# Kernel optimization log

Measured on AMD Instinct MI355X. Metric: run time of the kernel, lower is better.

Reference implementation:

```python
import jax, jax.numpy as jnp
import numpy as np

B, S, D, H, L = 8, 1024, 768, 12, 12
HD = D // H          # head dim 64
F = 4 * D            # mlp hidden 3072
N_SEG = 8            # ~images packed per sequence


def layer_norm(x, w, b, eps=1e-5):
    m = jnp.mean(x, axis=-1, keepdims=True)
    v = jnp.mean((x - m) ** 2, axis=-1, keepdims=True)
    return (x - m) / jnp.sqrt(v + eps) * w + b


def setup_inputs() -> dict:
    key = jax.random.key(0)
    ks = jax.random.split(key, 16)
    packed_tokens = jax.random.normal(ks[0], (B, S, D), dtype=jnp.float32)
    # block-diagonal mask from sorted segment ids (True = disallowed, torch bool-mask convention)
    seg = jnp.sort(jax.random.randint(ks[1], (S,), 0, N_SEG))
    attn_mask = seg[:, None] != seg[None, :]
    std = 0.02
    p = {
        'packed_tokens': packed_tokens,
        'attn_mask': attn_mask,
        'ln1_w': jnp.ones((L, D), jnp.float32),
        'ln1_b': jnp.zeros((L, D), jnp.float32),
        'wqkv': jax.random.normal(ks[2], (L, D, 3 * D), jnp.float32) * std,
        'bqkv': jnp.zeros((L, 3 * D), jnp.float32),
        'wo': jax.random.normal(ks[3], (L, D, D), jnp.float32) * std,
        'bo': jnp.zeros((L, D), jnp.float32),
        'ln2_w': jnp.ones((L, D), jnp.float32),
        'ln2_b': jnp.zeros((L, D), jnp.float32),
        'w1': jax.random.normal(ks[4], (L, D, F), jnp.float32) * std,
        'b1': jnp.zeros((L, F), jnp.float32),
        'w2': jax.random.normal(ks[5], (L, F, D), jnp.float32) * std,
        'b2': jnp.zeros((L, D), jnp.float32),
        'norm_w': jnp.ones((D,), jnp.float32),
        'norm_b': jnp.zeros((D,), jnp.float32),
    }
    return p


def attention(x, mask, wqkv, bqkv, wo, bo):
    qkv = x @ wqkv + bqkv                                  # [B,S,3D]
    q, k, v = jnp.split(qkv, 3, axis=-1)
    q = q.reshape(B, S, H, HD)
    k = k.reshape(B, S, H, HD)
    v = v.reshape(B, S, H, HD)
    scores = jnp.einsum('bqhd,bkhd->bhqk', q, k) / jnp.sqrt(jnp.asarray(HD, x.dtype))
    neg = jnp.asarray(jnp.finfo(scores.dtype).min, scores.dtype)
    scores = jnp.where(mask[None, None], neg, scores)
    probs = jax.nn.softmax(scores, axis=-1)
    out = jnp.einsum('bhqk,bkhd->bqhd', probs, v).reshape(B, S, D)
    return out @ wo + bo


def reference(packed_tokens, attn_mask, ln1_w, ln1_b, wqkv, bqkv, wo, bo,
              ln2_w, ln2_b, w1, b1, w2, b2, norm_w, norm_b):
    x = packed_tokens  # dropout = identity in eval
    for l in range(L):
        n = layer_norm(x, ln1_w[l], ln1_b[l])
        x = x + attention(n, attn_mask, wqkv[l], bqkv[l], wo[l], bo[l])
        n = layer_norm(x, ln2_w[l], ln2_b[l])
        h = jax.nn.gelu(n @ w1[l] + b1[l], approximate=False)
        x = x + h @ w2[l] + b2[l]
    return layer_norm(x, norm_w, norm_b)
```

## Files before the change

kernel.cpp:

```cpp
#include <hip/hip_runtime.h>
#include <hip/hip_bf16.h>
#include <math.h>

typedef __hip_bfloat16 bf16_t;
typedef _Float16 h16;
typedef _Float16 f16x8 __attribute__((ext_vector_type(8)));
typedef float f32x4 __attribute__((ext_vector_type(4)));

constexpr int B = 8;
constexpr int S = 1024;
constexpr int D = 768;
constexpr int H = 12;
constexpr int HD = 64;
constexpr int F = 3072;
constexpr int L = 12;
constexpr int T = B * S;


typedef const __attribute__((address_space(1))) void g_void;
typedef __attribute__((address_space(3))) void s_void;
#define GLD16(gp, lp) __builtin_amdgcn_global_load_lds((g_void*)(gp), (s_void*)(lp), 16, 0, 0)

__device__ __forceinline__ float ldf(const void* p, size_t i, int f32) {
    return f32 ? ((const float*)p)[i] : __bfloat162float(((const bf16_t*)p)[i]);
}

__device__ __forceinline__ int xcd_swz(int orig, int nwg) {
    return (orig & 7) * (nwg >> 3) + (orig >> 3);
}

__global__ void dtype_sniff_kernel(const uint32_t* __restrict__ w, int* __restrict__ meta) {
    if (threadIdx.x == 0) meta[1] = (w[0] == 0x3F800000u) ? 1 : 0;
}

__global__ __launch_bounds__(256) void mask_sniff_kernel(const uint32_t* __restrict__ mask,
                                                         int* __restrict__ meta) {
    __shared__ int firstw;
    if (threadIdx.x == 0) firstw = 1 << 30;
    __syncthreads();
    int idx = threadIdx.x;
    uint32_t v0 = mask[idx];
    uint32_t v1 = mask[256 + idx];
    uint32_t v2 = mask[512 + idx];
    uint32_t v3 = mask[768 + idx];
    int best = 1 << 30;
    if (v3) best = 768 + idx;
    if (v2) best = 512 + idx;
    if (v1) best = 256 + idx;
    if (v0) best = idx;
    atomicMin(&firstw, best);
    __syncthreads();
    if (threadIdx.x == 0) {
        int fi = firstw;
        meta[0] = (fi < (1 << 30) && mask[fi] == 1u) ? 1 : 0;
    }
}

__global__ __launch_bounds__(256) void rowrange_kernel(const void* __restrict__ mask,
                                                       int* __restrict__ meta) {
    int q = blockIdx.x;
    int f = meta[0];
    int lo = S, hi = -1;
    for (int j = threadIdx.x; j < S; j += 256) {
        int v = f ? ((const int*)mask)[(size_t)q * S + j]
                  : (int)((const unsigned char*)mask)[(size_t)q * S + j];
        if (v == 0) { lo = min(lo, j); hi = max(hi, j); }
    }
    for (int off = 32; off > 0; off >>= 1) {
        lo = min(lo, __shfl_xor(lo, off));
        hi = max(hi, __shfl_xor(hi, off));
    }
    __shared__ int slo[4], shi[4];
    int wv = threadIdx.x >> 6;
    if ((threadIdx.x & 63) == 0) { slo[wv] = lo; shi[wv] = hi; }
    __syncthreads();
    if (threadIdx.x == 0) {
        lo = min(min(slo[0], slo[1]), min(slo[2], slo[3]));
        hi = max(max(shi[0], shi[1]), max(shi[2], shi[3]));
        if (lo > hi) { lo = q; hi = q; }
        meta[16 + q] = lo;
        meta[16 + S + q] = hi;
    }
}

__global__ __launch_bounds__(256) void cast_kernel(const void* __restrict__ in,
                                                   const int* __restrict__ meta,
                                                   float* __restrict__ out, int n) {
    int f32 = meta[1];
    int i = blockIdx.x * 256 + threadIdx.x;
    if (i < n) out[i] = ldf(in, i, f32);
}

template <bool EXTERNAL>
__global__ __launch_bounds__(256) void ln_kernel(const float* __restrict__ x,
                                                 const void* __restrict__ w, size_t wo_,
                                                 const void* __restrict__ b, size_t bo_,
                                                 const int* __restrict__ meta,
                                                 void* __restrict__ out) {
    int f32 = meta[1];
    int t = blockIdx.x;
    int tid = threadIdx.x;
    __shared__ float xs[D];
    __shared__ float red[16];
    const float* xp = x + (size_t)t * D;

    float s = 0.f;
#pragma unroll
    for (int i = 0; i < 3; i++) {
        float v = xp[tid + i * 256];
        xs[tid + i * 256] = v;
        s += v;
    }
    for (int off = 32; off > 0; off >>= 1) s += __shfl_xor(s, off);
    int wv = tid >> 6, lane = tid & 63;
    if (lane == 0) red[wv] = s;
    __syncthreads();
    float mean = (red[0] + red[1] + red[2] + red[3]) * (1.0f / 768.0f);

    float s2 = 0.f;
#pragma unroll
    for (int i = 0; i < 3; i++) {
        float d = xs[tid + i * 256] - mean;
        s2 += d * d;
    }
    for (int off = 32; off > 0; off >>= 1) s2 += __shfl_xor(s2, off);
    if (lane == 0) red[8 + wv] = s2;
    __syncthreads();
    float var = (red[8] + red[9] + red[10] + red[11]) * (1.0f / 768.0f);
    float rstd = rsqrtf(var + 1e-5f);

#pragma unroll
    for (int i = 0; i < 3; i++) {
        int d = tid + i * 256;
        float v = (xs[d] - mean) * rstd * ldf(w, wo_ + d, f32) + ldf(b, bo_ + d, f32);
        size_t idx = (size_t)t * D + d;
        if (EXTERNAL) {
            if (f32) ((float*)out)[idx] = v;
            else ((bf16_t*)out)[idx] = __float2bfloat16(v);
        } else {
            ((h16*)out)[idx] = (h16)v;
        }
    }
}

__global__ __launch_bounds__(256) void wtrans_kernel(const void* __restrict__ W, size_t woff,
                                                     const int* __restrict__ meta,
                                                     h16* __restrict__ wt,
                                                     int K, int N) {
    int f32 = meta[1];
    __shared__ float tile[32][33];
    int n0 = blockIdx.x * 32, k0 = blockIdx.y * 32;
    int tx = threadIdx.x & 31, ty = threadIdx.x >> 5;
#pragma unroll
    for (int i = 0; i < 4; i++) {
        int k = ty + i * 8;
        tile[k][tx] = ldf(W, woff + (size_t)(k0 + k) * N + n0 + tx, f32);
    }
    __syncthreads();
#pragma unroll
    for (int i = 0; i < 4; i++) {
        int nn = ty + i * 8;
        wt[(size_t)(n0 + nn) * K + k0 + tx] = (h16)tile[tx][nn];
    }
}

template <bool GELU, bool ADD>
__global__ __launch_bounds__(256) void mgemm_kernel(const h16* __restrict__ A,
                                                    const h16* __restrict__ Bt,
                                                    const void* __restrict__ bias, size_t boff,
                                                    const int* __restrict__ meta,
                                                    void* __restrict__ C,
                                                    int M, int N, int K) {
    int f32 = meta[1];
    __shared__ h16 smem[4][128 * 32];
    int tid = threadIdx.x;
    int lane = tid & 63;
    int wv = tid >> 6;
    int wy = wv >> 1, wx = wv & 1;

    int nwg = gridDim.x * gridDim.y;
    int orig = blockIdx.y * gridDim.x + blockIdx.x;
    int fid = xcd_swz(orig, nwg);
    int n0 = (fid % gridDim.x) * 128;
    int m0 = (fid / gridDim.x) * 128;

    int row0 = tid >> 2;
    int row1 = 64 + row0;
    int kbs = ((tid & 3) ^ ((tid >> 3) & 3)) * 8;
    const h16* ag0 = A + (size_t)(m0 + row0) * K + kbs;
    const h16* ag1 = A + (size_t)(m0 + row1) * K + kbs;
    const h16* bg0 = Bt + (size_t)(n0 + row0) * K + kbs;
    const h16* bg1 = Bt + (size_t)(n0 + row1) * K + kbs;

    int arow = lane & 15;
    int akb = ((lane >> 4) ^ ((arow >> 1) & 3)) * 8;
    int aoff = (wy * 64 + arow) * 32 + akb;
    int boff2 = (wx * 64 + arow) * 32 + akb;

    f32x4 acc[4][4];
#pragma unroll
    for (int i = 0; i < 4; i++)
#pragma unroll
        for (int j = 0; j < 4; j++) acc[i][j] = (f32x4){0.f, 0.f, 0.f, 0.f};

    int nst = K >> 5;
    GLD16(ag0, &smem[0][(size_t)tid * 8]);
    GLD16(ag1, &smem[0][(size_t)(256 + tid) * 8]);
    GLD16(bg0, &smem[2][(size_t)tid * 8]);
    GLD16(bg1, &smem[2][(size_t)(256 + tid) * 8]);
    __syncthreads();

    int cur = 0;
    for (int t = 0; t < nst; ++t) {
        if (t + 1 < nst) {
            int nb = cur ^ 1;
            int off = (t + 1) * 32;
            GLD16(ag0 + off, &smem[nb][(size_t)tid * 8]);
            GLD16(ag1 + off, &smem[nb][(size_t)(256 + tid) * 8]);
            GLD16(bg0 + off, &smem[2 + nb][(size_t)tid * 8]);
            GLD16(bg1 + off, &smem[2 + nb][(size_t)(256 + tid) * 8]);
        }
        const h16* pa = &smem[cur][aoff];
        const h16* pb = &smem[2 + cur][boff2];
        f16x8 af[4], bf[4];
#pragma unroll
        for (int i = 0; i < 4; i++) af[i] = *(const f16x8*)(pa + i * 16 * 32);
#pragma unroll
        for (int j = 0; j < 4; j++) bf[j] = *(const f16x8*)(pb + j * 16 * 32);
#pragma unroll
        for (int i = 0; i < 4; i++)
#pragma unroll
            for (int j = 0; j < 4; j++)
                acc[i][j] = __builtin_amdgcn_mfma_f32_16x16x32_f16(af[i], bf[j], acc[i][j], 0, 0, 0);
        __syncthreads();
        cur ^= 1;
    }

    int col_local = wx * 64 + (lane & 15);
    int row_local = wy * 64 + (lane >> 4) * 4;
    if (ADD) {
#pragma unroll
        for (int j = 0; j < 4; j++) {
            int nn = n0 + col_local + j * 16;
            float bv = ldf(bias, boff + nn, f32);
#pragma unroll
            for (int i = 0; i < 4; i++) {
#pragma unroll
                for (int r = 0; r < 4; r++) {
                    int mm = m0 + row_local + i * 16 + r;
                    float v = acc[i][j][r] + bv;
                    ((float*)C)[(size_t)mm * N + nn] += v;
                }
            }
        }
    } else {
        h16* cst = &smem[0][0];
#pragma unroll
        for (int j = 0; j < 4; j++) {
            int cl = col_local + j * 16;
            float bv = ldf(bias, boff + n0 + cl, f32);
#pragma unroll
            for (int i = 0; i < 4; i++) {
#pragma unroll
                for (int r = 0; r < 4; r++) {
                    int rl = row_local + i * 16 + r;
                    float v = acc[i][j][r] + bv;
                    if (GELU) v = 0.5f * v * (1.0f + erff(v * 0.70710678118654752f));
                    cst[rl * 128 + (cl ^ ((rl & 7) << 3))] = (h16)v;
                }
            }
        }
        __syncthreads();
        int row = tid >> 1, cb = (tid & 1) * 64;
        h16* cg = (h16*)C + (size_t)(m0 + row) * N + n0 + cb;
#pragma unroll
        for (int u = 0; u < 8; u++) {
            int ce = cb + u * 8;
            f16x8 vv = *(const f16x8*)&cst[row * 128 + (ce ^ ((row & 7) << 3))];
            *(f16x8*)(cg + u * 8) = vv;
        }
    }
}

template <bool GELU, bool ADD>
__global__ __launch_bounds__(256) void gemm_kernel(const h16* __restrict__ A,
                                                   const void* __restrict__ W, size_t wo_,
                                                   const void* __restrict__ bias, size_t bo_,
                                                   const int* __restrict__ meta,
                                                   void* __restrict__ C,
                                                   int M, int N, int K) {
    int f32 = meta[1];
    __shared__ float As[16][65];
    __shared__ float Bs[16][65];
    int tid = threadIdx.y * 16 + threadIdx.x;
    int m0 = blockIdx.y * 64, n0 = blockIdx.x * 64;
    float c[4][4] = {};

    for (int k0 = 0; k0 < K; k0 += 16) {
#pragma unroll
        for (int i = 0; i < 4; i++) {
            int flat = tid + i * 256;
            int m = flat >> 4, k = flat & 15;
            As[k][m] = (float)A[(size_t)(m0 + m) * K + k0 + k];
        }
#pragma unroll
        for (int i = 0; i < 4; i++) {
            int flat = tid + i * 256;
            int k = flat >> 6, n = flat & 63;
            Bs[k][n] = ldf(W, wo_ + (size_t)(k0 + k) * N + n0 + n, f32);
        }
        __syncthreads();
#pragma unroll
        for (int kk = 0; kk < 16; kk++) {
            float a[4], bb[4];
#pragma unroll
            for (int i = 0; i < 4; i++) a[i] = As[kk][threadIdx.y * 4 + i];
#pragma unroll
            for (int j = 0; j < 4; j++) bb[j] = Bs[kk][threadIdx.x * 4 + j];
#pragma unroll
            for (int i = 0; i < 4; i++)
#pragma unroll
                for (int j = 0; j < 4; j++) c[i][j] += a[i] * bb[j];
        }
        __syncthreads();
    }

#pragma unroll
    for (int i = 0; i < 4; i++) {
        int m = m0 + threadIdx.y * 4 + i;
#pragma unroll
        for (int j = 0; j < 4; j++) {
            int n = n0 + threadIdx.x * 4 + j;
            float v = c[i][j] + ldf(bias, bo_ + n, f32);
            if (GELU) v = 0.5f * v * (1.0f + erff(v * 0.70710678118654752f));
            size_t idx = (size_t)m * N + n;
            if (ADD) ((float*)C)[idx] += v;
            else ((h16*)C)[idx] = (h16)v;
        }
    }
}

__global__ __launch_bounds__(256) void mattn_kernel(const h16* __restrict__ qkv,
                                                    const int* __restrict__ meta,
                                                    h16* __restrict__ ao) {
    const int* rowlo = meta + 16;
    const int* rowhi = meta + 16 + S;

    int nwg = gridDim.x * gridDim.y;
    int orig = blockIdx.y * gridDim.x + blockIdx.x;
    int fid = xcd_swz(orig, nwg);
    int bh = fid / gridDim.x;
    int q0 = (fid % gridDim.x) * 64;

    int b = bh / H, h = bh % H;
    int tid = threadIdx.x;
    int lane = tid & 63;
    int w = tid >> 6;
    int qw = q0 + w * 16;

    __shared__ h16 Vt[64 * 64];
    __shared__ h16 Ps[4][16 * 64];

    const size_t rs = 3 * D;
    const h16* base = qkv + (size_t)b * S * rs;

    int rl = rowlo[q0 + lane], rh = rowhi[q0 + lane];
    for (int off = 32; off > 0; off >>= 1) {
        rl = min(rl, __shfl_xor(rl, off));
        rh = max(rh, __shfl_xor(rh, off));
    }
    int c_lo = rl & ~63;
    int c_hi = rh + 1;

    int qrow = qw + (lane >> 4) * 4;
    int mlo[4], mhi[4];
#pragma unroll
    for (int r = 0; r < 4; r++) { mlo[r] = rowlo[qrow + r]; mhi[r] = rowhi[qrow + r]; }

    f16x8 qf[2];
    {
        const h16* qp = base + (size_t)(qw + (lane & 15)) * rs + h * 64 + (lane >> 4) * 8;
        qf[0] = *(const f16x8*)(qp);
        qf[1] = *(const f16x8*)(qp + 32);
    }

    float m_r[4], l_r[4];
    f32x4 o[4];
#pragma unroll
    for (int r = 0; r < 4; r++) { m_r[r] = -1e30f; l_r[r] = 0.f; }
#pragma unroll
    for (int jf = 0; jf < 4; jf++) o[jf] = (f32x4){0.f, 0.f, 0.f, 0.f};

    for (int c0 = c_lo; c0 < c_hi; c0 += 64) {
        {
            int k = tid & 63, d0 = (tid >> 6) * 16;
            const h16* vp = base + (size_t)(c0 + k) * rs + 2 * D + h * 64 + d0;
            f16x8 v0 = *(const f16x8*)vp;
            f16x8 v1 = *(const f16x8*)(vp + 8);
#pragma unroll
            for (int j = 0; j < 8; j++) {
                int d = d0 + j;
                Vt[(d * 64 + k) ^ ((d & 7) << 3)] = v0[j];
                d = d0 + 8 + j;
                Vt[(d * 64 + k) ^ ((d & 7) << 3)] = v1[j];
            }
        }

        f32x4 s[4];
#pragma unroll
        for (int jf = 0; jf < 4; jf++) {
            const h16* kp = base + (size_t)(c0 + jf * 16 + (lane & 15)) * rs + D + h * 64 + (lane >> 4) * 8;
            f16x8 kf0 = *(const f16x8*)kp;
            f16x8 kf1 = *(const f16x8*)(kp + 32);
            s[jf] = (f32x4){0.f, 0.f, 0.f, 0.f};
            s[jf] = __builtin_amdgcn_mfma_f32_16x16x32_f16(qf[0], kf0, s[jf], 0, 0, 0);
            s[jf] = __builtin_amdgcn_mfma_f32_16x16x32_f16(qf[1], kf1, s[jf], 0, 0, 0);
        }

        float pmax[4];
#pragma unroll
        for (int r = 0; r < 4; r++) pmax[r] = -3.0e38f;
#pragma unroll
        for (int jf = 0; jf < 4; jf++) {
            int k = c0 + jf * 16 + (lane & 15);
#pragma unroll
            for (int r = 0; r < 4; r++) {
                float v = (k < mlo[r] || k > mhi[r]) ? -3.0e38f : s[jf][r] * 0.125f;
                s[jf][r] = v;
                pmax[r] = fmaxf(pmax[r], v);
            }
        }
#pragma unroll
        for (int off = 1; off < 16; off <<= 1)
#pragma unroll
            for (int r = 0; r < 4; r++) pmax[r] = fmaxf(pmax[r], __shfl_xor(pmax[r], off));

        float scl[4];
#pragma unroll
        for (int r = 0; r < 4; r++) {
            float mn = fmaxf(m_r[r], pmax[r]);
            scl[r] = __expf(m_r[r] - mn);
            m_r[r] = mn;
            l_r[r] *= scl[r];
        }
#pragma unroll
        for (int jf = 0; jf < 4; jf++) {
#pragma unroll
            for (int r = 0; r < 4; r++) {
                float e = __expf(s[jf][r] - m_r[r]);
                l_r[r] += e;
                int q = (lane >> 4) * 4 + r;
                int k = jf * 16 + (lane & 15);
                Ps[w][(q * 64 + k) ^ ((q & 7) << 3)] = (h16)e;
            }
        }
#pragma unroll
        for (int jf = 0; jf < 4; jf++)
#pragma unroll
            for (int r = 0; r < 4; r++) o[jf][r] *= scl[r];

        __syncthreads();

        f16x8 pa0, pa1;
        {
            int q = lane & 15;
            int e0 = q * 64 + (lane >> 4) * 8;
            int e1 = q * 64 + 32 + (lane >> 4) * 8;
            pa0 = *(const f16x8*)&Ps[w][e0 ^ ((q & 7) << 3)];
            pa1 = *(const f16x8*)&Ps[w][e1 ^ ((q & 7) << 3)];
        }
#pragma unroll
        for (int jf = 0; jf < 4; jf++) {
            int d = jf * 16 + (lane & 15);
            int e0 = d * 64 + (lane >> 4) * 8;
            int e1 = d * 64 + 32 + (lane >> 4) * 8;
            f16x8 vb0 = *(const f16x8*)&Vt[e0 ^ ((d & 7) << 3)];
            f16x8 vb1 = *(const f16x8*)&Vt[e1 ^ ((d & 7) << 3)];
            o[jf] = __builtin_amdgcn_mfma_f32_16x16x32_f16(pa0, vb0, o[jf], 0, 0, 0);
            o[jf] = __builtin_amdgcn_mfma_f32_16x16x32_f16(pa1, vb1, o[jf], 0, 0, 0);
        }
        __syncthreads();
    }

#pragma unroll
    for (int off = 1; off < 16; off <<= 1)
#pragma unroll
        for (int r = 0; r < 4; r++) l_r[r] += __shfl_xor(l_r[r], off);
#pragma unroll
    for (int jf = 0; jf < 4; jf++) {
        int d = jf * 16 + (lane & 15);
#pragma unroll
        for (int r = 0; r < 4; r++) {
            float inv = (l_r[r] > 0.f) ? 1.0f / l_r[r] : 0.f;
            int q = qw + (lane >> 4) * 4 + r;
            ao[(size_t)(b * S + q) * D + h * 64 + d] = (h16)(o[jf][r] * inv);
        }
    }
}

__global__ __launch_bounds__(512) void attn_kernel(const h16* __restrict__ qkv,
                                                   const int* __restrict__ meta,
                                                   h16* __restrict__ ao) {
    const int* rowlo = meta + 16;
    const int* rowhi = meta + 16 + S;
    int bh = blockIdx.x;
    int b = bh / H, h = bh % H;
    int q0 = blockIdx.y * 8;
    int tid = threadIdx.x;
    int qr = tid >> 6;
    int lane = tid & 63;
    int q = q0 + qr;

    __shared__ float qs[8][64];
    __shared__ float sc[8][S];
    __shared__ float kv[64][65];

    const size_t rowstride = 3 * D;
    const h16* qkv_b = qkv + (size_t)b * S * rowstride;

    qs[qr][lane] = (float)qkv_b[(size_t)(q0 + qr) * rowstride + h * 64 + lane];

    int lo = rowlo[q], hi = rowhi[q];
    int blo = S, bhi = -1;
#pragma unroll
    for (int i = 0; i < 8; i++) {
        blo = min(blo, rowlo[q0 + i]);
        bhi = max(bhi, rowhi[q0 + i]);
    }
    int c_lo = (blo / 64) * 64;
    int c_hi = bhi + 1;
    int c_up = c_lo + ((c_hi - c_lo + 63) / 64) * 64;

    for (int c0 = c_lo; c0 < c_hi; c0 += 64) {
        __syncthreads();
#pragma unroll
        for (int i = 0; i < 8; i++) {
            int flat = tid + i * 512;
            int jj = flat >> 6, dd = flat & 63;
            kv[jj][dd] = (float)qkv_b[(size_t)(c0 + jj) * rowstride + D + h * 64 + dd];
        }
        __syncthreads();
        float acc = 0.f;
#pragma unroll
        for (int d = 0; d < 64; d++) acc += qs[qr][d] * kv[lane][d];
        int j = c0 + lane;
        bool msk = (j < lo) || (j > hi);
        sc[qr][j] = msk ? -3.0e38f : acc * 0.125f;
    }
    __syncthreads();

    float m = -3.4e38f;
    for (int j = c_lo + lane; j < c_up; j += 64) m = fmaxf(m, sc[qr][j]);
    for (int off = 32; off > 0; off >>= 1) m = fmaxf(m, __shfl_xor(m, off));
    float sum = 0.f;
    for (int j = c_lo + lane; j < c_up; j += 64) {
        float e = expf(sc[qr][j] - m);
        sc[qr][j] = e;
        sum += e;
    }
    for (int off = 32; off > 0; off >>= 1) sum += __shfl_xor(sum, off);
    float inv = (sum > 0.f) ? 1.0f / sum : 0.f;

    float out = 0.f;
    for (int c0 = c_lo; c0 < c_hi; c0 += 64) {
        __syncthreads();
#pragma unroll
        for (int i = 0; i < 8; i++) {
            int flat = tid + i * 512;
            int jj = flat >> 6, dd = flat & 63;
            kv[jj][dd] = (float)qkv_b[(size_t)(c0 + jj) * rowstride + 2 * D + h * 64 + dd];
        }
        __syncthreads();
#pragma unroll
        for (int jj = 0; jj < 64; jj++) out += sc[qr][c0 + jj] * kv[jj][lane];
    }
    out *= inv;
    ao[((size_t)(b * S + q)) * D + h * 64 + lane] = (h16)out;
}

__global__ __launch_bounds__(256) void sentinel_kernel(uint32_t* __restrict__ out, int nwords) {
    int i = blockIdx.x * 256 + threadIdx.x;
    if (i < nwords) out[i] = 0x3F803F80u;
}

extern "C" void kernel_launch(void* const* d_in, const int* in_sizes, int n_in,
                              void* d_out, int out_size, void* d_ws, size_t ws_size,
                              hipStream_t stream) {
    const void* packed = d_in[0];
    const void* mask   = d_in[1];
    const void* ln1w   = d_in[2];
    const void* ln1b   = d_in[3];
    const void* wqkv   = d_in[4];
    const void* bqkv   = d_in[5];
    const void* wo     = d_in[6];
    const void* bo     = d_in[7];
    const void* ln2w   = d_in[8];
    const void* ln2b   = d_in[9];
    const void* w1     = d_in[10];
    const void* b1     = d_in[11];
    const void* w2     = d_in[12];
    const void* b2     = d_in[13];
    const void* normw  = d_in[14];
    const void* normb  = d_in[15];

    size_t x_b   = (size_t)T * D * 4;
    size_t n_b   = (size_t)T * D * 2;
    size_t big_b = (size_t)T * F * 2;
    size_t need_old = 16384 + x_b + n_b + big_b;
    size_t wt_elems = (size_t)3 * D * D + (size_t)D * D + (size_t)D * F + (size_t)F * D;
    size_t need_new = need_old + wt_elems * 2 ;

    if (ws_size < need_old) {
        int nwords = out_size / 2;
        sentinel_kernel<<<(nwords + 255) / 256, 256, 0, stream>>>((uint32_t*)d_out, nwords);
        return;
    }

    int* meta = (int*)d_ws;
    float* x  = (float*)((char*)d_ws + 16384);
    h16* n    = (h16*)((char*)x + x_b);
    h16* big  = (h16*)((char*)n + n_b);

    dtype_sniff_kernel<<<1, 64, 0, stream>>>((const uint32_t*)ln1w, meta);
    mask_sniff_kernel<<<1, 256, 0, stream>>>((const uint32_t*)mask, meta);
    rowrange_kernel<<<S, 256, 0, stream>>>(mask, meta);
    cast_kernel<<<(T * D + 255) / 256, 256, 0, stream>>>(packed, meta, x, T * D);

    if (ws_size >= need_new) {
        h16* wts = (h16*)((char*)big + big_b);
        h16* qkvT = wts;
        h16* woT  = qkvT + (size_t)3 * D * D;
        h16* w1T  = woT + (size_t)D * D;
        h16* w2T  = w1T + (size_t)D * F;

        for (int l = 0; l < L; l++) {
            wtrans_kernel<<<dim3(3 * D / 32, D / 32), 256, 0, stream>>>(
                wqkv, (size_t)l * D * 3 * D, meta, qkvT, D, 3 * D);
            wtrans_kernel<<<dim3(D / 32, D / 32), 256, 0, stream>>>(
                wo, (size_t)l * D * D, meta, woT, D, D);
            wtrans_kernel<<<dim3(F / 32, D / 32), 256, 0, stream>>>(
                w1, (size_t)l * D * F, meta, w1T, D, F);
            wtrans_kernel<<<dim3(D / 32, F / 32), 256, 0, stream>>>(
                w2, (size_t)l * F * D, meta, w2T, F, D);

            ln_kernel<false><<<T, 256, 0, stream>>>(x, ln1w, (size_t)l * D, ln1b, (size_t)l * D, meta, n);
            mgemm_kernel<false, false><<<dim3(3 * D / 128, T / 128), 256, 0, stream>>>(
                n, qkvT, bqkv, (size_t)l * 3 * D, meta, big, T, 3 * D, D);
            mattn_kernel<<<dim3(S / 64, B * H), 256, 0, stream>>>(big, meta, n);
            mgemm_kernel<false, true><<<dim3(D / 128, T / 128), 256, 0, stream>>>(
                n, woT, bo, (size_t)l * D, meta, x, T, D, D);
            ln_kernel<false><<<T, 256, 0, stream>>>(x, ln2w, (size_t)l * D, ln2b, (size_t)l * D, meta, n);
            mgemm_kernel<true, false><<<dim3(F / 128, T / 128), 256, 0, stream>>>(
                n, w1T, b1, (size_t)l * F, meta, big, T, F, D);
            mgemm_kernel<false, true><<<dim3(D / 128, T / 128), 256, 0, stream>>>(
                big, w2T, b2, (size_t)l * D, meta, x, T, D, F);
        }
    } else {
        dim3 thr(16, 16);
        for (int l = 0; l < L; l++) {
            ln_kernel<false><<<T, 256, 0, stream>>>(x, ln1w, (size_t)l * D, ln1b, (size_t)l * D, meta, n);
            gemm_kernel<false, false><<<dim3(3 * D / 64, T / 64), thr, 0, stream>>>(
                n, wqkv, (size_t)l * D * 3 * D, bqkv, (size_t)l * 3 * D, meta, big, T, 3 * D, D);
            attn_kernel<<<dim3(B * H, S / 8), 512, 0, stream>>>(big, meta, n);
            gemm_kernel<false, true><<<dim3(D / 64, T / 64), thr, 0, stream>>>(
                n, wo, (size_t)l * D * D, bo, (size_t)l * D, meta, x, T, D, D);
            ln_kernel<false><<<T, 256, 0, stream>>>(x, ln2w, (size_t)l * D, ln2b, (size_t)l * D, meta, n);
            gemm_kernel<true, false><<<dim3(F / 64, T / 64), thr, 0, stream>>>(
                n, w1, (size_t)l * D * F, b1, (size_t)l * F, meta, big, T, F, D);
            gemm_kernel<false, true><<<dim3(D / 64, T / 64), thr, 0, stream>>>(
                big, w2, (size_t)l * F * D, b2, (size_t)l * D, meta, x, T, D, F);
        }
    }
    ln_kernel<true><<<T, 256, 0, stream>>>(x, normw, 0, normb, 0, meta, d_out);
}
```

Baseline: 4.016 ms.

## Widen GEMM N-tile to 256 for QKV/MLP1 and pre-transpose all layer weights

Templates the MFMA GEMM on the number of 16-wide N fragments so the QKV and FC1 GEMMs use 128x256 tiles (more accumulators per wave, more reuse of A fragments), with the epilogue staged through LDS in 128-column passes. It also transposes all layers' weights up front into a larger workspace region when space allows, instead of transposing per layer between dependent kernels. The wider tiles raise register pressure and halve the grid for those GEMMs, which may reduce occupancy; the upfront transpose needs more workspace.

```diff
diff --git a/kernel.cpp b/kernel.cpp
--- a/kernel.cpp
+++ b/kernel.cpp
@@ -164,15 +164,18 @@
     }
 }
 
-template <bool GELU, bool ADD>
+template <bool GELU, bool ADD, int NF>
 __global__ __launch_bounds__(256) void mgemm_kernel(const h16* __restrict__ A,
                                                     const h16* __restrict__ Bt,
                                                     const void* __restrict__ bias, size_t boff,
                                                     const int* __restrict__ meta,
                                                     void* __restrict__ C,
                                                     int M, int N, int K) {
+    constexpr int BN = NF * 32;
+    constexpr int ASZ = 128 * 32;
+    constexpr int BSZ = BN * 32;
     int f32 = meta[1];
-    __shared__ h16 smem[4][128 * 32];
+    __shared__ h16 smem[2 * ASZ + 2 * BSZ];
     int tid = threadIdx.x;
     int lane = tid & 63;
     int wv = tid >> 6;
@@ -181,33 +184,31 @@
     int nwg = gridDim.x * gridDim.y;
     int orig = blockIdx.y * gridDim.x + blockIdx.x;
     int fid = xcd_swz(orig, nwg);
-    int n0 = (fid % gridDim.x) * 128;
+    int n0 = (fid % gridDim.x) * BN;
     int m0 = (fid / gridDim.x) * 128;
 
     int row0 = tid >> 2;
-    int row1 = 64 + row0;
     int kbs = ((tid & 3) ^ ((tid >> 3) & 3)) * 8;
-    const h16* ag0 = A + (size_t)(m0 + row0) * K + kbs;
-    const h16* ag1 = A + (size_t)(m0 + row1) * K + kbs;
-    const h16* bg0 = Bt + (size_t)(n0 + row0) * K + kbs;
-    const h16* bg1 = Bt + (size_t)(n0 + row1) * K + kbs;
+    const h16* ag = A + (size_t)(m0 + row0) * K + kbs;
+    const h16* bg = Bt + (size_t)(n0 + row0) * K + kbs;
 
     int arow = lane & 15;
     int akb = ((lane >> 4) ^ ((arow >> 1) & 3)) * 8;
     int aoff = (wy * 64 + arow) * 32 + akb;
-    int boff2 = (wx * 64 + arow) * 32 + akb;
-
-    f32x4 acc[4][4];
+    int boff2 = (wx * (NF * 16) + arow) * 32 + akb;
+
+    f32x4 acc[4][NF];
 #pragma unroll
     for (int i = 0; i < 4; i++)
 #pragma unroll
-        for (int j = 0; j < 4; j++) acc[i][j] = (f32x4){0.f, 0.f, 0.f, 0.f};
+        for (int j = 0; j < NF; j++) acc[i][j] = (f32x4){0.f, 0.f, 0.f, 0.f};
 
     int nst = K >> 5;
-    GLD16(ag0, &smem[0][(size_t)tid * 8]);
-    GLD16(ag1, &smem[0][(size_t)(256 + tid) * 8]);
-    GLD16(bg0, &smem[2][(size_t)tid * 8]);
-    GLD16(bg1, &smem[2][(size_t)(256 + tid) * 8]);
+    GLD16(ag, smem + (size_t)tid * 8);
+    GLD16(ag + (size_t)64 * K, smem + (size_t)(256 + tid) * 8);
+#pragma unroll
+    for (int i = 0; i < NF / 2; i++)
+        GLD16(bg + (size_t)(i * 64) * K, smem + 2 * ASZ + (size_t)(i * 256 + tid) * 8);
     __syncthreads();
 
     int cur = 0;
@@ -215,69 +216,81 @@
         if (t + 1 < nst) {
             int nb = cur ^ 1;
             int off = (t + 1) * 32;
-            GLD16(ag0 + off, &smem[nb][(size_t)tid * 8]);
-            GLD16(ag1 + off, &smem[nb][(size_t)(256 + tid) * 8]);
-            GLD16(bg0 + off, &smem[2 + nb][(size_t)tid * 8]);
-            GLD16(bg1 + off, &smem[2 + nb][(size_t)(256 + tid) * 8]);
-        }
-        const h16* pa = &smem[cur][aoff];
-        const h16* pb = &smem[2 + cur][boff2];
-        f16x8 af[4], bf[4];
+            GLD16(ag + off, smem + (size_t)nb * ASZ + (size_t)tid * 8);
+            GLD16(ag + (size_t)64 * K + off, smem + (size_t)nb * ASZ + (size_t)(256 + tid) * 8);
+#pragma unroll
+            for (int i = 0; i < NF / 2; i++)
+                GLD16(bg + (size_t)(i * 64) * K + off,
+                      smem + 2 * ASZ + (size_t)nb * BSZ + (size_t)(i * 256 + tid) * 8);
+        }
+        const h16* pa = smem + (size_t)cur * ASZ + aoff;
+        const h16* pb = smem + 2 * ASZ + (size_t)cur * BSZ + boff2;
+        f16x8 af[4];
 #pragma unroll
         for (int i = 0; i < 4; i++) af[i] = *(const f16x8*)(pa + i * 16 * 32);
 #pragma unroll
-        for (int j = 0; j < 4; j++) bf[j] = *(const f16x8*)(pb + j * 16 * 32);
-#pragma unroll
-        for (int i = 0; i < 4; i++)
-#pragma unroll
-            for (int j = 0; j < 4; j++)
-                acc[i][j] = __builtin_amdgcn_mfma_f32_16x16x32_f16(af[i], bf[j], acc[i][j], 0, 0, 0);
+        for (int jh = 0; jh < NF / 4; jh++) {
+            f16x8 bf[4];
+#pragma unroll
+            for (int jj = 0; jj < 4; jj++) bf[jj] = *(const f16x8*)(pb + (jh * 4 + jj) * 16 * 32);
+#pragma unroll
+            for (int i = 0; i < 4; i++)
+#pragma unroll
+                for (int jj = 0; jj < 4; jj++)
+                    acc[i][jh * 4 + jj] =
+                        __builtin_amdgcn_mfma_f32_16x16x32_f16(af[i], bf[jj], acc[i][jh * 4 + jj], 0, 0, 0);
+        }
         __syncthreads();
         cur ^= 1;
     }
 
-    int col_local = wx * 64 + (lane & 15);
     int row_local = wy * 64 + (lane >> 4) * 4;
     if (ADD) {
 #pragma unroll
-        for (int j = 0; j < 4; j++) {
-            int nn = n0 + col_local + j * 16;
+        for (int j = 0; j < NF; j++) {
+            int nn = n0 + wx * (NF * 16) + (lane & 15) + j * 16;
             float bv = ldf(bias, boff + nn, f32);
 #pragma unroll
             for (int i = 0; i < 4; i++) {
 #pragma unroll
                 for (int r = 0; r < 4; r++) {
                     int mm = m0 + row_local + i * 16 + r;
-                    float v = acc[i][j][r] + bv;
-                    ((float*)C)[(size_t)mm * N + nn] += v;
+                    ((float*)C)[(size_t)mm * N + nn] += acc[i][j][r] + bv;
                 }
             }
         }
     } else {
-        h16* cst = &smem[0][0];
-#pragma unroll
-        for (int j = 0; j < 4; j++) {
-            int cl = col_local + j * 16;
-            float bv = ldf(bias, boff + n0 + cl, f32);
-#pragma unroll
-            for (int i = 0; i < 4; i++) {
-#pragma unroll
-                for (int r = 0; r < 4; r++) {
-                    int rl = row_local + i * 16 + r;
-                    float v = acc[i][j][r] + bv;
-                    if (GELU) v = 0.5f * v * (1.0f + erff(v * 0.70710678118654752f));
-                    cst[rl * 128 + (cl ^ ((rl & 7) << 3))] = (h16)v;
+        constexpr int NPASS = BN / 128;
+        h16* cst = smem;
+#pragma unroll
+        for (int p = 0; p < NPASS; p++) {
+            if (p > 0) __syncthreads();
+#pragma unroll
+            for (int j = 0; j < NF; j++) {
+                if (((wx * NF + j) >> 3) != p) continue;
+                int cl = wx * (NF * 16) + (lane & 15) + j * 16;
+                float bv = ldf(bias, boff + n0 + cl, f32);
+                int cll = cl & 127;
+#pragma unroll
+                for (int i = 0; i < 4; i++) {
+#pragma unroll
+                    for (int r = 0; r < 4; r++) {
+                        int rl = row_local + i * 16 + r;
+                        float v = acc[i][j][r] + bv;
+                        if (GELU) v = 0.5f * v * (1.0f + erff(v * 0.70710678118654752f));
+                        cst[rl * 128 + (cll ^ ((rl & 7) << 3))] = (h16)v;
+                    }
                 }
             }
-        }
-        __syncthreads();
-        int row = tid >> 1, cb = (tid & 1) * 64;
-        h16* cg = (h16*)C + (size_t)(m0 + row) * N + n0 + cb;
-#pragma unroll
-        for (int u = 0; u < 8; u++) {
-            int ce = cb + u * 8;
-            f16x8 vv = *(const f16x8*)&cst[row * 128 + (ce ^ ((row & 7) << 3))];
-            *(f16x8*)(cg + u * 8) = vv;
+            __syncthreads();
+            int row = tid >> 1, cb = (tid & 1) * 64;
+            h16* cg = (h16*)C + (size_t)(m0 + row) * N + n0 + p * 128 + cb;
+#pragma unroll
+            for (int u = 0; u < 8; u++) {
+                int ce = cb + u * 8;
+                f16x8 vv = *(const f16x8*)&cst[row * 128 + (ce ^ ((row & 7) << 3))];
+                *(f16x8*)(cg + u * 8) = vv;
+            }
         }
     }
 }
@@ -608,7 +621,8 @@
     size_t big_b = (size_t)T * F * 2;
     size_t need_old = 16384 + x_b + n_b + big_b;
     size_t wt_elems = (size_t)3 * D * D + (size_t)D * D + (size_t)D * F + (size_t)F * D;
-    size_t need_new = need_old + wt_elems * 2 ;
+    size_t need_new = need_old + wt_elems * 2;
+    size_t need_all = need_old + wt_elems * 2 * L;
 
     if (ws_size < need_old) {
         int nwords = out_size / 2;
@@ -628,31 +642,50 @@
 
     if (ws_size >= need_new) {
         h16* wts = (h16*)((char*)big + big_b);
-        h16* qkvT = wts;
-        h16* woT  = qkvT + (size_t)3 * D * D;
-        h16* w1T  = woT + (size_t)D * D;
-        h16* w2T  = w1T + (size_t)D * F;
+        bool all = (ws_size >= need_all);
+
+        if (all) {
+            for (int l = 0; l < L; l++) {
+                h16* base = wts + (size_t)l * wt_elems;
+                wtrans_kernel<<<dim3(3 * D / 32, D / 32), 256, 0, stream>>>(
+                    wqkv, (size_t)l * D * 3 * D, meta, base, D, 3 * D);
+                wtrans_kernel<<<dim3(D / 32, D / 32), 256, 0, stream>>>(
+                    wo, (size_t)l * D * D, meta, base + (size_t)3 * D * D, D, D);
+                wtrans_kernel<<<dim3(F / 32, D / 32), 256, 0, stream>>>(
+                    w1, (size_t)l * D * F, meta, base + (size_t)4 * D * D, D, F);
+                wtrans_kernel<<<dim3(D / 32, F / 32), 256, 0, stream>>>(
+                    w2, (size_t)l * F * D, meta, base + (size_t)4 * D * D + (size_t)D * F, F, D);
+            }
+        }
 
         for (int l = 0; l < L; l++) {
-            wtrans_kernel<<<dim3(3 * D / 32, D / 32), 256, 0, stream>>>(
-                wqkv, (size_t)l * D * 3 * D, meta, qkvT, D, 3 * D);
-            wtrans_kernel<<<dim3(D / 32, D / 32), 256, 0, stream>>>(
-                wo, (size_t)l * D * D, meta, woT, D, D);
-            wtrans_kernel<<<dim3(F / 32, D / 32), 256, 0, stream>>>(
-                w1, (size_t)l * D * F, meta, w1T, D, F);
-            wtrans_kernel<<<dim3(D / 32, F / 32), 256, 0, stream>>>(
-                w2, (size_t)l * F * D, meta, w2T, F, D);
+            h16* base = all ? wts + (size_t)l * wt_elems : wts;
+            h16* qkvT = base;
+            h16* woT  = base + (size_t)3 * D * D;
+            h16* w1T  = base + (size_t)4 * D * D;
+            h16* w2T  = base + (size_t)4 * D * D + (size_t)D * F;
+
+            if (!all) {
+                wtrans_kernel<<<dim3(3 * D / 32, D / 32), 256, 0, stream>>>(
+                    wqkv, (size_t)l * D * 3 * D, meta, qkvT, D, 3 * D);
+                wtrans_kernel<<<dim3(D / 32, D / 32), 256, 0, stream>>>(
+                    wo, (size_t)l * D * D, meta, woT, D, D);
+                wtrans_kernel<<<dim3(F / 32, D / 32), 256, 0, stream>>>(
+                    w1, (size_t)l * D * F, meta, w1T, D, F);
+                wtrans_kernel<<<dim3(D / 32, F / 32), 256, 0, stream>>>(
+                    w2, (size_t)l * F * D, meta, w2T, F, D);
+            }
 
             ln_kernel<false><<<T, 256, 0, stream>>>(x, ln1w, (size_t)l * D, ln1b, (size_t)l * D, meta, n);
-            mgemm_kernel<false, false><<<dim3(3 * D / 128, T / 128), 256, 0, stream>>>(
+            mgemm_kernel<false, false, 8><<<dim3(3 * D / 256, T / 128), 256, 0, stream>>>(
                 n, qkvT, bqkv, (size_t)l * 3 * D, meta, big, T, 3 * D, D);
             mattn_kernel<<<dim3(S / 64, B * H), 256, 0, stream>>>(big, meta, n);
-            mgemm_kernel<false, true><<<dim3(D / 128, T / 128), 256, 0, stream>>>(
+            mgemm_kernel<false, true, 4><<<dim3(D / 128, T / 128), 256, 0, stream>>>(
                 n, woT, bo, (size_t)l * D, meta, x, T, D, D);
             ln_kernel<false><<<T, 256, 0, stream>>>(x, ln2w, (size_t)l * D, ln2b, (size_t)l * D, meta, n);
-            mgemm_kernel<true, false><<<dim3(F / 128, T / 128), 256, 0, stream>>>(
+            mgemm_kernel<true, false, 8><<<dim3(F / 256, T / 128), 256, 0, stream>>>(
                 n, w1T, b1, (size_t)l * F, meta, big, T, F, D);
-            mgemm_kernel<false, true><<<dim3(D / 128, T / 128), 256, 0, stream>>>(
+            mgemm_kernel<false, true, 4><<<dim3(D / 128, T / 128), 256, 0, stream>>>(
                 big, w2T, b2, (size_t)l * D, meta, x, T, D, F);
         }
     } else {
```

New measurement: 5.605 ms. 1.4x slower.
